# Performance work log

Measured on AMD Instinct MI355X. Metric: run time of the kernel, lower is better.

The kernel has to match this reference:

```python
import jax, jax.numpy as jnp
import numpy as np

B, L = 8, 2048
AMP, ANG = 48, 16
H = 4
AQK, GQK = 12, 6   # amp/ang qk head dims
AV, GV = 12, 6     # amp/ang v head dims
LOOKBACK = 100


def setup_inputs() -> dict:
    key = jax.random.key(0)
    ks = jax.random.split(key, 16)
    def w(k, i, o):
        # kaiming-uniform-ish scale; stored [in, out] so forward is x @ W
        bound = 1.0 / np.sqrt(i)
        return jax.random.uniform(k, (i, o), jnp.float32, -bound, bound)
    return dict(
        x_ang=jax.random.normal(ks[0], (B, L, 2 * ANG), jnp.float32),
        x_amp=jax.random.normal(ks[1], (B, L, AMP), jnp.float32),
        Wq_amp=w(ks[2], AMP, H * AQK),
        Wk_amp=w(ks[3], AMP, H * AQK),
        Wv_amp=w(ks[4], AMP, H * AV),
        Wq_ang_r=w(ks[5], ANG, H * GQK),
        Wq_ang_i=w(ks[6], ANG, H * GQK),
        Wk_ang_r=w(ks[7], ANG, H * GQK),
        Wk_ang_i=w(ks[8], ANG, H * GQK),
        Wv_ang_r=w(ks[9], ANG, H * GV),
        Wv_ang_i=w(ks[10], ANG, H * GV),
        Wout_amp=w(ks[11], H * AV, AMP),
        bout_amp=jax.random.uniform(ks[12], (AMP,), jnp.float32, -0.1, 0.1),
        Wout_ang_r=w(ks[13], H * GV, ANG),
        Wout_ang_i=w(ks[14], H * GV, ANG),
    )


def _clin(xr, xi, Wr, Wi):
    # complex linear: (xr + i xi) @ (Wr + i Wi)
    return xr @ Wr - xi @ Wi, xr @ Wi + xi @ Wr


def reference(x_ang, x_amp, Wq_amp, Wk_amp, Wv_amp,
              Wq_ang_r, Wq_ang_i, Wk_ang_r, Wk_ang_i,
              Wv_ang_r, Wv_ang_i, Wout_amp, bout_amp,
              Wout_ang_r, Wout_ang_i):
    Bb, Ll, CA = x_ang.shape
    ang_r, ang_i = jnp.split(x_ang, 2, axis=-1)

    def heads(x, hd):  # [B,L,H*hd] -> [B,H,L,hd]
        return x.reshape(Bb, Ll, H, hd).transpose(0, 2, 1, 3)

    q_amp = heads(x_amp @ Wq_amp, AQK)
    k_amp = heads(x_amp @ Wk_amp, AQK)
    qar, qai = _clin(ang_r, ang_i, Wq_ang_r, Wq_ang_i)
    kar, kai = _clin(ang_r, ang_i, Wk_ang_r, Wk_ang_i)
    q = jnp.concatenate([heads(qar, GQK), heads(qai, GQK), q_amp], axis=-1)  # [B,H,L,24]
    k = jnp.concatenate([heads(kar, GQK), heads(kai, GQK), k_amp], axis=-1)

    v_amp = heads(x_amp @ Wv_amp, AV)
    var, vai = _clin(ang_r, ang_i, Wv_ang_r, Wv_ang_i)
    v = jnp.concatenate([heads(var, GV), heads(vai, GV), v_amp], axis=-1)  # [B,H,L,24]

    scale = 1.0 / jnp.sqrt(jnp.asarray(q.shape[-1], q.dtype))
    scores = jnp.einsum('bhqd,bhkd->bhqk', q, k) * scale
    idx = jnp.arange(Ll)
    valid = (idx[None, :] <= idx[:, None]) & (idx[None, :] >= idx[:, None] - (LOOKBACK - 1))
    mask = jnp.where(valid, jnp.asarray(0.0, scores.dtype), jnp.finfo(scores.dtype).min)
    attn = jax.nn.softmax(scores + mask, axis=-1)
    out = jnp.einsum('bhqk,bhkd->bhqd', attn, v)  # [B,H,L,24]

    o_ang_r, o_ang_i, o_amp = jnp.split(out, [GV, 2 * GV], axis=-1)

    def merge(x):  # [B,H,L,hd] -> [B,L,H*hd]
        return x.transpose(0, 2, 1, 3).reshape(Bb, Ll, -1)

    out_amp = merge(o_amp) @ Wout_amp + bout_amp
    out_ang_r, out_ang_i = _clin(merge(o_ang_r), merge(o_ang_i), Wout_ang_r, Wout_ang_i)
    return (out_ang_r, out_ang_i, out_amp)
```

## Files before the change

kernel.cpp:

```cpp
#include <hip/hip_runtime.h>
#include <hip/hip_bf16.h>

constexpr int B = 8;
constexpr int L = 2048;
constexpr int ANG = 16;
constexpr int AMP = 48;
constexpr int H = 4;
constexpr int AQK = 12, GQK = 6;
constexpr int AV = 12, GV = 6;
constexpr int HD = 2 * GQK + AQK;
constexpr int LOOKBACK = 100;

constexpr int NTOK = B * L;

constexpr int QKV_AMP_JOBS = NTOK * 48;
constexpr int QKV_ANG_JOBS = NTOK * 72;
constexpr int QKV_AMP_BLOCKS = QKV_AMP_JOBS / 256;
constexpr int QKV_ANG_BLOCKS = QKV_ANG_JOBS / 256;

__global__ __launch_bounds__(256) void qkv2_kernel(
    const float* __restrict__ x_ang, const float* __restrict__ x_amp,
    const float* __restrict__ Wq_amp, const float* __restrict__ Wk_amp,
    const float* __restrict__ Wv_amp,
    const float* __restrict__ Wq_ang_r, const float* __restrict__ Wq_ang_i,
    const float* __restrict__ Wk_ang_r, const float* __restrict__ Wk_ang_i,
    const float* __restrict__ Wv_ang_r, const float* __restrict__ Wv_ang_i,
    float* __restrict__ q, float* __restrict__ k, float* __restrict__ v)
{
    int bid = blockIdx.x;
    if (bid < QKV_AMP_BLOCKS) {
        int g   = bid * 256 + threadIdx.x;
        int col = g % 48;
        int tok = g / 48;

        const float4* xm4 = (const float4*)(x_amp + (size_t)tok * AMP);
        float x[48];
        #pragma unroll
        for (int i = 0; i < 12; i++) {
            float4 t = xm4[i];
            x[4*i+0] = t.x; x[4*i+1] = t.y; x[4*i+2] = t.z; x[4*i+3] = t.w;
        }

        float aq = 0.f, ak = 0.f, av = 0.f;
        #pragma unroll
        for (int i = 0; i < 48; i++) {
            aq += x[i] * Wq_amp[i * 48 + col];
            ak += x[i] * Wk_amp[i * 48 + col];
            av += x[i] * Wv_amp[i * 48 + col];
        }

        int b = tok / L, l = tok % L;
        int h = col / 12, ca = col % 12;
        size_t o = (((size_t)b * H + h) * L + l) * HD + (2 * GQK) + ca;
        q[o] = aq; k[o] = ak; v[o] = av;
    } else {
        int g     = (bid - QKV_AMP_BLOCKS) * 256 + threadIdx.x;
        int j     = g % 72;
        int tok   = g / 72;
        int mat   = j / 24;
        int combo = j % 24;
        int h     = combo / 6, dd = combo % 6;

        const float4* xa4 = (const float4*)(x_ang + (size_t)tok * (2 * ANG));
        float xr[16], xi[16];
        #pragma unroll
        for (int i = 0; i < 4; i++) {
            float4 t = xa4[i];
            xr[4*i+0] = t.x; xr[4*i+1] = t.y; xr[4*i+2] = t.z; xr[4*i+3] = t.w;
            float4 u = xa4[4 + i];
            xi[4*i+0] = u.x; xi[4*i+1] = u.y; xi[4*i+2] = u.z; xi[4*i+3] = u.w;
        }

        const float* Wr = (mat == 0) ? Wq_ang_r : (mat == 1) ? Wk_ang_r : Wv_ang_r;
        const float* Wi = (mat == 0) ? Wq_ang_i : (mat == 1) ? Wk_ang_i : Wv_ang_i;

        float orr = 0.f, oii = 0.f;
        #pragma unroll
        for (int i = 0; i < 16; i++) {
            float wr = Wr[i * 24 + combo], wi = Wi[i * 24 + combo];
            orr += xr[i] * wr - xi[i] * wi;
            oii += xr[i] * wi + xi[i] * wr;
        }

        float* dst = (mat == 0) ? q : (mat == 1) ? k : v;
        int b = tok / L, l = tok % L;
        size_t base = (((size_t)b * H + h) * L + l) * HD;
        dst[base + dd]       = orr;
        dst[base + GQK + dd] = oii;
    }
}

constexpr int TQ   = 128;
constexpr int MAXK = TQ + LOOKBACK - 1;
constexpr int KP   = 28;

__global__ __launch_bounds__(256) void attn2_kernel(
    const float* __restrict__ q, const float* __restrict__ k,
    const float* __restrict__ v, float* __restrict__ att)
{
    constexpr int NT = L / TQ;
    int bh = blockIdx.x / NT;
    int qt = blockIdx.x % NT;
    int q0 = qt * TQ;
    int kmin = q0 - (LOOKBACK - 1); if (kmin < 0) kmin = 0;
    int nrows = (q0 + TQ - 1) - kmin + 1;

    __shared__ float Ks[MAXK][KP];
    __shared__ float Vs[MAXK][KP];
    __shared__ float Pm[TQ], Ps[TQ];
    __shared__ float Po[TQ][25];

    {
        const float4* kb4 = (const float4*)(k + ((size_t)bh * L + kmin) * HD);
        const float4* vb4 = (const float4*)(v + ((size_t)bh * L + kmin) * HD);
        int nch = nrows * 6;
        for (int c = threadIdx.x; c < nch; c += 256) {
            int r = c / 6, s = c % 6;
            *(float4*)&Ks[r][s * 4] = kb4[c];
            *(float4*)&Vs[r][s * 4] = vb4[c];
        }
    }
    __syncthreads();

    int qlocal = threadIdx.x & (TQ - 1);
    int group  = threadIdx.x >> 7;
    int qi = q0 + qlocal;

    float qr[HD];
    {
        const float4* qp4 = (const float4*)(q + ((size_t)bh * L + qi) * HD);
        #pragma unroll
        for (int i = 0; i < 6; i++) {
            float4 t = qp4[i];
            qr[4*i+0] = t.x; qr[4*i+1] = t.y; qr[4*i+2] = t.z; qr[4*i+3] = t.w;
        }
    }

    const float scale = 0.2041241452319315f;
    float m = -3.0e38f, s = 0.f;
    float o[HD];
    #pragma unroll
    for (int d = 0; d < HD; d++) o[d] = 0.f;

    int j0 = qi - (LOOKBACK - 1); if (j0 < 0) j0 = 0;
    for (int j = j0 + group; j <= qi; j += 2) {
        int r = j - kmin;
        float sc = 0.f;
        #pragma unroll
        for (int d = 0; d < HD; d++) sc += qr[d] * Ks[r][d];
        sc *= scale;
        float mn   = fmaxf(m, sc);
        float corr = __expf(m - mn);
        float p    = __expf(sc - mn);
        s = s * corr + p;
        #pragma unroll
        for (int d = 0; d < HD; d++) o[d] = o[d] * corr + p * Vs[r][d];
        m = mn;
    }

    if (group == 0) {
        Pm[qlocal] = m; Ps[qlocal] = s;
        #pragma unroll
        for (int d = 0; d < HD; d++) Po[qlocal][d] = o[d];
    }
    __syncthreads();
    if (group == 1) {
        float m2 = Pm[qlocal], s2 = Ps[qlocal];
        float mm = fmaxf(m, m2);
        float c1 = __expf(m - mm), c2 = __expf(m2 - mm);
        float inv = 1.f / (s * c1 + s2 * c2);
        float* op = att + ((size_t)bh * L + qi) * HD;
        #pragma unroll
        for (int d = 0; d < HD; d++)
            op[d] = (o[d] * c1 + Po[qlocal][d] * c2) * inv;
    }
}

constexpr int PAMP_JOBS   = NTOK * 48;
constexpr int PANG_JOBS   = NTOK * 16;
constexpr int PAMP_BLOCKS = PAMP_JOBS / 256;
constexpr int PANG_BLOCKS = PANG_JOBS / 256;

__global__ __launch_bounds__(256) void proj2_kernel(
    const float* __restrict__ att,
    const float* __restrict__ Wout_amp, const float* __restrict__ bout_amp,
    const float* __restrict__ Wout_ang_r, const float* __restrict__ Wout_ang_i,
    float* __restrict__ out)
{
    constexpr size_t ANG_OUT = (size_t)NTOK * ANG;
    int bid = blockIdx.x;

    if (bid < PAMP_BLOCKS) {
        int g   = bid * 256 + threadIdx.x;
        int col = g % 48;
        int tok = g / 48;
        int b = tok / L, l = tok % L;

        float a[48];
        #pragma unroll
        for (int h = 0; h < H; h++) {
            const float4* ap4 = (const float4*)(att + (((size_t)b * H + h) * L + l) * HD + 2 * GV);
            #pragma unroll
            for (int i = 0; i < 3; i++) {
                float4 t = ap4[i];
                a[h*12 + 4*i+0] = t.x; a[h*12 + 4*i+1] = t.y;
                a[h*12 + 4*i+2] = t.z; a[h*12 + 4*i+3] = t.w;
            }
        }
        float acc = bout_amp[col];
        #pragma unroll
        for (int i = 0; i < 48; i++)
            acc += a[i] * Wout_amp[i * AMP + col];
        out[2 * ANG_OUT + (size_t)tok * AMP + col] = acc;
    } else {
        int g   = (bid - PAMP_BLOCKS) * 256 + threadIdx.x;
        int col = g % 16;
        int tok = g / 16;
        int b = tok / L, l = tok % L;

        float ar[24], ai[24];
        #pragma unroll
        for (int h = 0; h < H; h++) {
            const float4* ap4 = (const float4*)(att + (((size_t)b * H + h) * L + l) * HD);
            float4 t0 = ap4[0], t1 = ap4[1], t2 = ap4[2];
            ar[h*6+0] = t0.x; ar[h*6+1] = t0.y; ar[h*6+2] = t0.z; ar[h*6+3] = t0.w;
            ar[h*6+4] = t1.x; ar[h*6+5] = t1.y;
            ai[h*6+0] = t1.z; ai[h*6+1] = t1.w;
            ai[h*6+2] = t2.x; ai[h*6+3] = t2.y; ai[h*6+4] = t2.z; ai[h*6+5] = t2.w;
        }
        float accr = 0.f, acci = 0.f;
        #pragma unroll
        for (int i = 0; i < 24; i++) {
            float wr = Wout_ang_r[i * ANG + col], wi = Wout_ang_i[i * ANG + col];
            accr += ar[i] * wr - ai[i] * wi;
            acci += ar[i] * wi + ai[i] * wr;
        }
        out[(size_t)tok * ANG + col]           = accr;
        out[ANG_OUT + (size_t)tok * ANG + col] = acci;
    }
}

extern "C" void kernel_launch(void* const* d_in, const int* in_sizes, int n_in,
                              void* d_out, int out_size, void* d_ws, size_t ws_size,
                              hipStream_t stream)
{
    const float* x_ang      = (const float*)d_in[0];
    const float* x_amp      = (const float*)d_in[1];
    const float* Wq_amp     = (const float*)d_in[2];
    const float* Wk_amp     = (const float*)d_in[3];
    const float* Wv_amp     = (const float*)d_in[4];
    const float* Wq_ang_r   = (const float*)d_in[5];
    const float* Wq_ang_i   = (const float*)d_in[6];
    const float* Wk_ang_r   = (const float*)d_in[7];
    const float* Wk_ang_i   = (const float*)d_in[8];
    const float* Wv_ang_r   = (const float*)d_in[9];
    const float* Wv_ang_i   = (const float*)d_in[10];
    const float* Wout_amp   = (const float*)d_in[11];
    const float* bout_amp   = (const float*)d_in[12];
    const float* Wout_ang_r = (const float*)d_in[13];
    const float* Wout_ang_i = (const float*)d_in[14];

    float* out = (float*)d_out;
    float* ws  = (float*)d_ws;

    const size_t N = (size_t)B * H * L * HD;
    float* q   = ws;
    float* k   = ws + N;
    float* v   = ws + 2 * N;
    float* att = ws + 3 * N;

    qkv2_kernel<<<QKV_AMP_BLOCKS + QKV_ANG_BLOCKS, 256, 0, stream>>>(
        x_ang, x_amp, Wq_amp, Wk_amp, Wv_amp,
        Wq_ang_r, Wq_ang_i, Wk_ang_r, Wk_ang_i, Wv_ang_r, Wv_ang_i,
        q, k, v);

    attn2_kernel<<<B * H * (L / TQ), 256, 0, stream>>>(q, k, v, att);

    proj2_kernel<<<PAMP_BLOCKS + PANG_BLOCKS, 256, 0, stream>>>(
        att, Wout_amp, bout_amp, Wout_ang_r, Wout_ang_i, out);
}
```

Measured before the change: 153.2 us.

## Split attention keys over four thread groups with swizzled float4 shared tiles

The attention kernel now processes 64 queries per block, and four thread groups each take every fourth key instead of two groups over 128 queries. K/V tiles are stored as float4 with an XOR swizzle to avoid LDS bank conflicts on row-strided reads, and the partial softmax states of all four groups are merged cooperatively, with vectorized float4 stores. The aim is shorter serial key loops per thread and more blocks to fill the GPU. The cost is more redundant K/V halo loading per block and a larger merge step.

```diff
diff --git a/kernel.cpp b/kernel.cpp
--- a/kernel.cpp
+++ b/kernel.cpp
@@ -90,25 +90,26 @@
     }
 }
 
-constexpr int TQ   = 128;
-constexpr int MAXK = TQ + LOOKBACK - 1;
-constexpr int KP   = 28;
-
-__global__ __launch_bounds__(256) void attn2_kernel(
+constexpr int TQA    = 64;
+constexpr int GROUPS = 4;
+constexpr int MAXKA  = TQA + LOOKBACK - 1;
+
+__global__ __launch_bounds__(256) void attn3_kernel(
     const float* __restrict__ q, const float* __restrict__ k,
     const float* __restrict__ v, float* __restrict__ att)
 {
-    constexpr int NT = L / TQ;
+    constexpr int NT = L / TQA;
     int bh = blockIdx.x / NT;
     int qt = blockIdx.x % NT;
-    int q0 = qt * TQ;
+    int q0 = qt * TQA;
     int kmin = q0 - (LOOKBACK - 1); if (kmin < 0) kmin = 0;
-    int nrows = (q0 + TQ - 1) - kmin + 1;
-
-    __shared__ float Ks[MAXK][KP];
-    __shared__ float Vs[MAXK][KP];
-    __shared__ float Pm[TQ], Ps[TQ];
-    __shared__ float Po[TQ][25];
+    int nrows = (q0 + TQA - 1) - kmin + 1;
+
+    __shared__ float4 Ks4[MAXKA][8];
+    __shared__ float4 Vs4[MAXKA][8];
+    __shared__ float  Pm[GROUPS][TQA];
+    __shared__ float  Ps[GROUPS][TQA];
+    __shared__ float4 Po4[GROUPS][TQA][6];
 
     {
         const float4* kb4 = (const float4*)(k + ((size_t)bh * L + kmin) * HD);
@@ -116,63 +117,94 @@
         int nch = nrows * 6;
         for (int c = threadIdx.x; c < nch; c += 256) {
             int r = c / 6, s = c % 6;
-            *(float4*)&Ks[r][s * 4] = kb4[c];
-            *(float4*)&Vs[r][s * 4] = vb4[c];
+            int slot = s ^ (r & 7);
+            Ks4[r][slot] = kb4[c];
+            Vs4[r][slot] = vb4[c];
         }
     }
     __syncthreads();
 
-    int qlocal = threadIdx.x & (TQ - 1);
-    int group  = threadIdx.x >> 7;
+    int qlocal = threadIdx.x & (TQA - 1);
+    int group  = threadIdx.x >> 6;
     int qi = q0 + qlocal;
 
-    float qr[HD];
+    float4 qr4[6];
     {
         const float4* qp4 = (const float4*)(q + ((size_t)bh * L + qi) * HD);
         #pragma unroll
-        for (int i = 0; i < 6; i++) {
-            float4 t = qp4[i];
-            qr[4*i+0] = t.x; qr[4*i+1] = t.y; qr[4*i+2] = t.z; qr[4*i+3] = t.w;
-        }
+        for (int s = 0; s < 6; s++) qr4[s] = qp4[s];
     }
 
     const float scale = 0.2041241452319315f;
-    float m = -3.0e38f, s = 0.f;
-    float o[HD];
+    float m = -3.0e38f, ss = 0.f;
+    float4 o4[6];
     #pragma unroll
-    for (int d = 0; d < HD; d++) o[d] = 0.f;
+    for (int s = 0; s < 6; s++) { o4[s].x = 0.f; o4[s].y = 0.f; o4[s].z = 0.f; o4[s].w = 0.f; }
 
     int j0 = qi - (LOOKBACK - 1); if (j0 < 0) j0 = 0;
-    for (int j = j0 + group; j <= qi; j += 2) {
-        int r = j - kmin;
+    for (int j = j0 + group; j <= qi; j += GROUPS) {
+        int r  = j - kmin;
+        int rx = r & 7;
         float sc = 0.f;
         #pragma unroll
-        for (int d = 0; d < HD; d++) sc += qr[d] * Ks[r][d];
+        for (int s = 0; s < 6; s++) {
+            float4 kk = Ks4[r][s ^ rx];
+            sc += qr4[s].x * kk.x + qr4[s].y * kk.y + qr4[s].z * kk.z + qr4[s].w * kk.w;
+        }
         sc *= scale;
         float mn   = fmaxf(m, sc);
         float corr = __expf(m - mn);
         float p    = __expf(sc - mn);
-        s = s * corr + p;
-        #pragma unroll
-        for (int d = 0; d < HD; d++) o[d] = o[d] * corr + p * Vs[r][d];
+        ss = ss * corr + p;
+        #pragma unroll
+        for (int s = 0; s < 6; s++) {
+            float4 vv = Vs4[r][s ^ rx];
+            o4[s].x = o4[s].x * corr + p * vv.x;
+            o4[s].y = o4[s].y * corr + p * vv.y;
+            o4[s].z = o4[s].z * corr + p * vv.z;
+            o4[s].w = o4[s].w * corr + p * vv.w;
+        }
         m = mn;
     }
 
-    if (group == 0) {
-        Pm[qlocal] = m; Ps[qlocal] = s;
-        #pragma unroll
-        for (int d = 0; d < HD; d++) Po[qlocal][d] = o[d];
-    }
+    Pm[group][qlocal] = m;
+    Ps[group][qlocal] = ss;
+    #pragma unroll
+    for (int s = 0; s < 6; s++) Po4[group][qlocal][s] = o4[s];
     __syncthreads();
-    if (group == 1) {
-        float m2 = Pm[qlocal], s2 = Ps[qlocal];
-        float mm = fmaxf(m, m2);
-        float c1 = __expf(m - mm), c2 = __expf(m2 - mm);
-        float inv = 1.f / (s * c1 + s2 * c2);
-        float* op = att + ((size_t)bh * L + qi) * HD;
-        #pragma unroll
-        for (int d = 0; d < HD; d++)
-            op[d] = (o[d] * c1 + Po[qlocal][d] * c2) * inv;
+
+    {
+        int qq    = threadIdx.x & 63;
+        int chunk = threadIdx.x >> 6;
+        float m0 = Pm[0][qq], m1 = Pm[1][qq], m2 = Pm[2][qq], m3 = Pm[3][qq];
+        float mm = fmaxf(fmaxf(m0, m1), fmaxf(m2, m3));
+        float c0 = __expf(m0 - mm), c1 = __expf(m1 - mm);
+        float c2 = __expf(m2 - mm), c3 = __expf(m3 - mm);
+        float denom = Ps[0][qq] * c0 + Ps[1][qq] * c1 + Ps[2][qq] * c2 + Ps[3][qq] * c3;
+        float inv = 1.f / denom;
+
+        float4* op4 = (float4*)(att + ((size_t)bh * L + q0 + qq) * HD);
+
+        int s = chunk;
+        {
+            float4 a0 = Po4[0][qq][s], a1 = Po4[1][qq][s], a2 = Po4[2][qq][s], a3 = Po4[3][qq][s];
+            float4 acc;
+            acc.x = (a0.x * c0 + a1.x * c1 + a2.x * c2 + a3.x * c3) * inv;
+            acc.y = (a0.y * c0 + a1.y * c1 + a2.y * c2 + a3.y * c3) * inv;
+            acc.z = (a0.z * c0 + a1.z * c1 + a2.z * c2 + a3.z * c3) * inv;
+            acc.w = (a0.w * c0 + a1.w * c1 + a2.w * c2 + a3.w * c3) * inv;
+            op4[s] = acc;
+        }
+        if (chunk < 2) {
+            s = chunk + 4;
+            float4 a0 = Po4[0][qq][s], a1 = Po4[1][qq][s], a2 = Po4[2][qq][s], a3 = Po4[3][qq][s];
+            float4 acc;
+            acc.x = (a0.x * c0 + a1.x * c1 + a2.x * c2 + a3.x * c3) * inv;
+            acc.y = (a0.y * c0 + a1.y * c1 + a2.y * c2 + a3.y * c3) * inv;
+            acc.z = (a0.z * c0 + a1.z * c1 + a2.z * c2 + a3.z * c3) * inv;
+            acc.w = (a0.w * c0 + a1.w * c1 + a2.w * c2 + a3.w * c3) * inv;
+            op4[s] = acc;
+        }
     }
 }
 
@@ -274,7 +306,7 @@
         Wq_ang_r, Wq_ang_i, Wk_ang_r, Wk_ang_i, Wv_ang_r, Wv_ang_i,
         q, k, v);
 
-    attn2_kernel<<<B * H * (L / TQ), 256, 0, stream>>>(q, k, v, att);
+    attn3_kernel<<<B * H * (L / TQA), 256, 0, stream>>>(q, k, v, att);
 
     proj2_kernel<<<PAMP_BLOCKS + PANG_BLOCKS, 256, 0, stream>>>(
         att, Wout_amp, bout_amp, Wout_ang_r, Wout_ang_i, out);
```

Result: no change. 154.5 us (+0.9%).
